# Performance work log

Measured on AMD Instinct MI355X. Metric: run time of the kernel, lower is better.

The kernel has to match this reference:

```python
import jax, jax.numpy as jnp
import numpy as np

N, E, H, NH, HD = 16384, 131072, 128, 8, 16
CUTOFF = 5.0
PATCH = H // 2  # 64, aggregation_custom effective patch dim


def setup_inputs() -> dict:
    key = jax.random.key(0)
    ks = jax.random.split(key, 24)
    w = lambda k, s: (jax.random.normal(k, s, dtype=jnp.float32) * 0.05)
    d = jax.random.normal(ks[5], (E, 3), dtype=jnp.float32)
    d = d / (jnp.linalg.norm(d, axis=-1, keepdims=True) + 1e-8)  # unit directions
    return {
        "x": jax.random.normal(ks[0], (N, H), dtype=jnp.float32),
        "vec": jax.random.normal(ks[1], (N, 3, H), dtype=jnp.float32),
        "edge_index": jax.random.randint(ks[2], (2, E), 0, N),
        "r_ij": jax.random.uniform(ks[3], (E,), dtype=jnp.float32) * CUTOFF,
        "f_ij": jax.random.normal(ks[4], (E, H), dtype=jnp.float32),
        "d_ij": d,
        "ln_g": jnp.ones((H,), jnp.float32), "ln_b": jnp.zeros((H,), jnp.float32),
        "Wq": w(ks[6], (H, H)), "bq": jnp.zeros((H,), jnp.float32),
        "Wk": w(ks[7], (H, H)), "bk": jnp.zeros((H,), jnp.float32),
        "Wv": w(ks[8], (H, H)), "bv": jnp.zeros((H,), jnp.float32),
        "Wdk": w(ks[9], (H, H)), "bdk": jnp.zeros((H,), jnp.float32),
        "Wdv": w(ks[10], (H, H)), "bdv": jnp.zeros((H,), jnp.float32),
        "Wvec": w(ks[11], (3 * H, H)),
        "Ws": w(ks[12], (2 * H, H)), "bs": jnp.zeros((2 * H,), jnp.float32),
        "Wo": w(ks[13], (3 * H, H)), "bo": jnp.zeros((3 * H,), jnp.float32),
        "Wf": w(ks[14], (H, H)), "bf": jnp.zeros((H,), jnp.float32),
        "Wwsrc": w(ks[15], (H, H)), "Wwtrg": w(ks[16], (H, H)),
        "Wagg": w(ks[17], (H, PATCH)),  # fc_all: Linear(64 -> 128, no bias)
        "agg_param": jnp.full((1,), 1e-5, dtype=jnp.float32),
    }


def _cutoff(r):
    return 0.5 * (jnp.cos(jnp.pi * r / CUTOFF) + 1.0) * (r < CUTOFF).astype(r.dtype)


def _vector_rejection(v, d):
    # v: [E,3,H], d: [E,3]
    proj = (v * d[:, :, None]).sum(axis=1, keepdims=True)  # [E,1,H]
    return v - proj * d[:, :, None]


def reference(x, vec, edge_index, r_ij, f_ij, d_ij, ln_g, ln_b,
              Wq, bq, Wk, bk, Wv, bv, Wdk, bdk, Wdv, bdv, Wvec,
              Ws, bs, Wo, bo, Wf, bf, Wwsrc, Wwtrg, Wagg, agg_param):
    silu = jax.nn.silu
    n = x.shape[0]
    # LayerNorm on x; VecLayerNorm with norm_type='none', trainable=False is identity
    mu = x.mean(-1, keepdims=True)
    var = ((x - mu) ** 2).mean(-1, keepdims=True)
    xn = (x - mu) / jnp.sqrt(var + 1e-5) * ln_g + ln_b

    q = (xn @ Wq.T + bq).reshape(n, NH, HD)
    k = (xn @ Wk.T + bk).reshape(n, NH, HD)
    v = (xn @ Wv.T + bv).reshape(n, NH, HD)
    dk = silu(f_ij @ Wdk.T + bdk).reshape(-1, NH, HD)
    dv = silu(f_ij @ Wdv.T + bdv).reshape(-1, NH, HD)

    vec1, vec2, vec3 = jnp.split(jnp.einsum('nch,oh->nco', vec, Wvec), 3, axis=-1)
    vec_dot = (vec1 * vec2).sum(axis=1)  # [N,H]

    src, dst = edge_index[0], edge_index[1]  # j, i
    # --- message ---
    attn = (q[dst] * k[src] * dk).sum(-1)                      # [E,NH]
    attn = silu(attn) * _cutoff(r_ij)[:, None]
    vmsg = (v[src] * dv * attn[:, :, None]).reshape(-1, H)     # [E,H]
    s1, s2 = jnp.split(silu(vmsg @ Ws.T + bs), 2, axis=1)
    vec_msg = vec[src] * s1[:, None, :] + s2[:, None, :] * d_ij[:, :, None]  # [E,3,H]

    # --- aggregation_custom on scalar messages ---
    e = vmsg.reshape(-1, 2, PATCH)                 # [E,2,64]
    ex = jnp.clip(jnp.einsum('epd,od->epo', e, Wagg), 0.0, 1.0)  # [E,2,128]
    gated = jnp.concatenate([(e * ex[:, :, :PATCH]).sum(1),
                             (e * ex[:, :, PATCH:]).sum(1)], axis=-1)  # [E,128]
    x_orig = jax.ops.segment_sum(vmsg, dst, num_segments=n)
    x_gate = jax.ops.segment_sum(gated, dst, num_segments=n)
    x_agg = jnp.abs(agg_param) * x_gate + x_orig
    vec_agg = jax.ops.segment_sum(vec_msg.reshape(-1, 3 * H), dst, num_segments=n).reshape(n, 3, H)

    # --- update ---
    o1, o2, o3 = jnp.split(x_agg @ Wo.T + bo, 3, axis=1)
    dx = vec_dot * o2 + o3
    dvec = vec3 * o1[:, None, :] + vec_agg

    # --- edge_update ---
    w1 = _vector_rejection(jnp.einsum('ech,oh->eco', vec[dst], Wwtrg), d_ij)
    w2 = _vector_rejection(jnp.einsum('ech,oh->eco', vec[src], Wwsrc), -d_ij)
    w_dot = (w1 * w2).sum(axis=1)  # [E,H]
    df_ij = silu(f_ij @ Wf.T + bf) * w_dot
    return dx, dvec, df_ij
```

## Files before the change

### kernel.cpp

```cpp
#include <hip/hip_runtime.h>

#define NN 16384
#define NE 131072
#define HH 128

typedef unsigned short u16;
typedef unsigned int u32;
typedef __attribute__((ext_vector_type(8))) short short8;
typedef __attribute__((ext_vector_type(4))) float f32x4;
typedef __attribute__((ext_vector_type(2))) float f32x2;
typedef __attribute__((ext_vector_type(2))) u32 u32x2;

__device__ __forceinline__ float b2f(u16 u){ u32 i=((u32)u)<<16; float f; __builtin_memcpy(&f,&i,4); return f; }
__device__ __forceinline__ u16 f2b(float f){ u32 i; __builtin_memcpy(&i,&f,4); u32 r=(i+0x7fffu+((i>>16)&1u))>>16; return (u16)r; }
__device__ __forceinline__ float blo(u32 v){ return b2f((u16)(v&0xffffu)); }
__device__ __forceinline__ float bhi(u32 v){ return b2f((u16)(v>>16)); }
__device__ __forceinline__ u32 pk(float a, float b){ return (u32)f2b(a) | ((u32)f2b(b)<<16); }
__device__ __forceinline__ float siluf(float x){ return x/(1.f+__expf(-x)); }

#define SW8(b) ((b) ^ ((((b)>>8)&7)<<4))
#define SW9(b) ((b) ^ ((((b)>>9)&7)<<4))

#define PBASE 58720256u
enum : unsigned {
  O_Wq=PBASE+0, O_Wk=PBASE+16384, O_Wv=PBASE+32768, O_Wdk=PBASE+49152,
  O_Wdv=PBASE+65536, O_Wf=PBASE+81920, O_Wwsrc=PBASE+98304, O_Wwtrg=PBASE+114688,
  O_Wvec=PBASE+131072, O_Ws=PBASE+180224, O_Wo=PBASE+212992, O_Wagg=PBASE+262144,
  O_bq=PBASE+270336, O_bk=PBASE+270464, O_bv=PBASE+270592, O_bdk=PBASE+270720,
  O_bdv=PBASE+270848, O_bs=PBASE+270976, O_bo=PBASE+271232, O_bf=PBASE+271616,
  O_lng=PBASE+271744, O_lnb=PBASE+271872, O_agg=PBASE+272000
};
#define CNT_OFF 117985280u
#define CUR_OFF 118050816u
#define SE_OFF  118116352u

struct Seg { const float* s; u32 off; u32 n; };
struct Pack { Seg d[25]; int cnt; };

__global__ __launch_bounds__(256) void k_cvt(Pack p, u16* __restrict__ base){
  int tid = blockIdx.x*blockDim.x + threadIdx.x;
  int stride = gridDim.x*blockDim.x;
  for (int s=0; s<p.cnt; ++s){
    const float* src = p.d[s].s;
    u16* dst = base + p.d[s].off;
    int n = (int)p.d[s].n, n4 = n>>2;
    const f32x4* s4 = (const f32x4*)src;
    for (int i=tid; i<n4; i+=stride){
      f32x4 v = s4[i];
      u32x2 o; o[0] = pk(v[0], v[1]); o[1] = pk(v[2], v[3]);
      *(u32x2*)(dst + 4*(size_t)i) = o;
    }
    for (int i = n4*4 + tid; i < n; i += stride) dst[i] = f2b(src[i]);
  }
}

__global__ __launch_bounds__(256) void k_hist(const int* __restrict__ ei, int* __restrict__ cnt){
  int e = blockIdx.x*256 + threadIdx.x;
  atomicAdd(&cnt[ei[NE + e]], 1);
}
__global__ __launch_bounds__(1024) void k_scan(const int* __restrict__ cnt, int* __restrict__ cur){
  __shared__ int part[1024];
  int t = threadIdx.x;
  int base = t*16;
  int local[16]; int s = 0;
#pragma unroll
// ... 5 lines not shown
    __syncthreads();
    part[t] += v;
    __syncthreads();
  }
  int run = (t>0) ? part[t-1] : 0;
#pragma unroll
  for (int k=0;k<16;++k){ cur[base+k] = run; run += local[k]; }
}
__global__ __launch_bounds__(256) void k_place(const int* __restrict__ ei, int* __restrict__ cur,
                                               int* __restrict__ se){
  int e = blockIdx.x*256 + threadIdx.x;
  int p = atomicAdd(&cur[ei[NE + e]], 1);
  se[p] = e;
}

template<int NK>
__device__ __forceinline__ f32x4 mm16(const u16* A, int lda, const u16* W, int ldw, f32x4 acc){
  int lane = threadIdx.x & 63;
  const u16* pa = A + (lane & 15)*lda + ((lane>>4)<<3);
  const u16* pw = W + (lane & 15)*ldw + ((lane>>4)<<3);
#pragma unroll
  for (int kc = 0; kc < NK; ++kc){
    short8 a = *(const short8*)(pa + kc*32);
    short8 b = *(const short8*)(pw + kc*32);
    acc = __builtin_amdgcn_mfma_f32_16x16x32_bf16(a, b, acc, 0, 0, 0);
  }
  return acc;
}

__global__ __launch_bounds__(256) void k_ln(const float* __restrict__ x, const u16* __restrict__ pb,
                                            u16* __restrict__ xn){
  int wid = threadIdx.x>>6, lane = threadIdx.x & 63;
  int n = blockIdx.x*4 + wid;
  f32x2 v = *(const f32x2*)(x + (size_t)n*HH + 2*lane);
  float a0 = v[0], a1 = v[1];
  float s = a0 + a1;
#pragma unroll
  for (int m=32; m; m>>=1) s += __shfl_xor(s, m);
  float mu = s*(1.f/128.f);
  float d0 = a0-mu, d1 = a1-mu;
  float vs = d0*d0 + d1*d1;
#pragma unroll
  for (int m=32; m; m>>=1) vs += __shfl_xor(vs, m);
  float rs = rsqrtf(vs*(1.f/128.f) + 1e-5f);
  u32 gg = *(const u32*)(pb + O_lng + 2*lane);
  u32 bb = *(const u32*)(pb + O_lnb + 2*lane);
  *(u32*)(xn + (size_t)n*HH + 2*lane) = pk(d0*rs*blo(gg)+blo(bb), d1*rs*bhi(gg)+bhi(bb));
}

__global__ __launch_bounds__(256) void k_gemm_qkv(const u16* __restrict__ xn,
    const u16* __restrict__ pb, u16* __restrict__ qkv){
  int wid = threadIdx.x>>6, lane = threadIdx.x & 63;
  int ct = blockIdx.y*4 + wid;
  int r0 = blockIdx.x*16;
  unsigned wo, bo_;
  if (ct < 8)      { wo = O_Wq; bo_ = O_bq; }
  else if (ct <16) { wo = O_Wk; bo_ = O_bk; }
  else             { wo = O_Wv; bo_ = O_bv; }
  int c0 = (ct & 7)*16;
  f32x4 acc = {0,0,0,0};
  acc = mm16<4>(xn + (size_t)r0*HH, HH, pb + wo + c0*HH, HH, acc);
  int col = ct*16 + (lane & 15);
  float bb = b2f(pb[bo_ + c0 + (lane&15)]);
#pragma unroll
  for (int j=0;j<4;++j){
    int r = r0 + ((lane>>4)<<2) + j;
    qkv[(size_t)r*384 + col] = f2b(acc[j] + bb);
  }
}

__global__ __launch_bounds__(256) void k_gemm_vec(const float* __restrict__ vecf,
    const u16* __restrict__ pb,
    u16* __restrict__ v12, u16* __restrict__ vec3, u16* __restrict__ Y){
  __shared__ u16 At[16*128];
  int tid = threadIdx.x, wid = tid>>6, lane = tid & 63;
  int r0 = blockIdx.x*16;
  {
    const float* src = vecf + (size_t)r0*HH;
    for (int i = tid*4; i < 2048; i += 1024){
      f32x4 v = *(const f32x4*)(src + i);
      u32x2 o; o[0] = pk(v[0], v[1]); o[1] = pk(v[2], v[3]);
      *(u32x2*)(At + i) = o;
    }
  }
  __syncthreads();
  for (int ct = wid; ct < 40; ct += 4){
    unsigned wo; int wc0;
    if (ct < 24)      { wo = O_Wvec;  wc0 = ct*16; }
    else if (ct < 32) { wo = O_Wwsrc; wc0 = (ct-24)*16; }
    else              { wo = O_Wwtrg; wc0 = (ct-32)*16; }
    f32x4 acc = {0,0,0,0};
    acc = mm16<4>(At, HH, pb + wo + wc0*HH, HH, acc);
    u16* dst; int ldc, dc0;
    if (ct < 16)      { dst = v12;  ldc = 256; dc0 = ct*16; }
    else if (ct < 24) { dst = vec3; ldc = 128; dc0 = (ct-16)*16; }
    else if (ct < 32) { dst = Y;    ldc = 256; dc0 = (ct-24)*16; }
    else              { dst = Y;    ldc = 256; dc0 = (ct-32)*16 + 128; }
    int col = dc0 + (lane & 15);
#pragma unroll
    for (int j=0;j<4;++j){
      int r = r0 + ((lane>>4)<<2) + j;
      dst[(size_t)r*ldc + col] = f2b(acc[j]);
    }
  }
}

__global__ __launch_bounds__(256) void k_edge(const float* __restrict__ f_ij,
    const u16* __restrict__ pb,
    const u16* __restrict__ qkv, const u16* __restrict__ Y,
    const int* __restrict__ ei, const int* __restrict__ se,
    const float* __restrict__ r_ij, const float* __restrict__ d_ij,
    const float* __restrict__ vecf, const float* __restrict__ aggf,
    float* __restrict__ df, float* __restrict__ xacc, float* __restrict__ vacc){
  __shared__ u16 fs[64*128];
  __shared__ u16 g2s[64*256];
  char* fsb  = (char*)fs;
  char* g2b  = (char*)g2s;
// ... 1 lines not shown
  int t0 = blockIdx.x*64;
  int ereg=0, dreg=0, sreg=0;
  if (lane < 16){
    ereg = se[t0 + wid*16 + lane];
    dreg = ei[NE + ereg];
    sreg = ei[ereg];
  }
#pragma unroll
  for (int pass=0; pass<8; ++pass){
    int idx = pass*256 + lane*4;
    int rloc = idx >> 7, col = idx & 127;
    int er = __shfl(ereg, rloc);
    f32x4 v = *(const f32x4*)(f_ij + (size_t)er*HH + col);
    u32x2 o; o[0]=pk(v[0],v[1]); o[1]=pk(v[2],v[3]);
    int b = (wid*16 + rloc)*256 + col*2;
    *(u32x2*)(fsb + SW8(b)) = o;
  }
  {
    int arow = wid*16 + (lane&15);
    int ab = arow*256 + ((lane>>4)<<4);
    short8 a0 = *(const short8*)(fsb + SW8(ab));
    short8 a1 = *(const short8*)(fsb + SW8(ab + 64));
    short8 a2 = *(const short8*)(fsb + SW8(ab + 128));
    short8 a3 = *(const short8*)(fsb + SW8(ab + 192));
    for (int ct=0; ct<16; ++ct){
      unsigned wo  = (ct<8) ? O_Wdk : O_Wdv;
      unsigned bo_ = (ct<8) ? O_bdk : O_bdv;
      int c0 = (ct&7)*16;
      const u16* pw = pb + wo + (size_t)(c0 + (lane&15))*HH + ((lane>>4)<<3);
      f32x4 acc = {0,0,0,0};
      acc = __builtin_amdgcn_mfma_f32_16x16x32_bf16(a0, *(const short8*)(pw),      acc, 0,0,0);
      acc = __builtin_amdgcn_mfma_f32_16x16x32_bf16(a1, *(const short8*)(pw + 32), acc, 0,0,0);
      acc = __builtin_amdgcn_mfma_f32_16x16x32_bf16(a2, *(const short8*)(pw + 64), acc, 0,0,0);
      acc = __builtin_amdgcn_mfma_f32_16x16x32_bf16(a3, *(const short8*)(pw + 96), acc, 0,0,0);
      float bb = b2f(pb[bo_ + c0 + (lane&15)]);
#pragma unroll
      for (int j=0;j<4;++j){
        int r = wid*16 + ((lane>>4)<<2) + j;
        int b = r*512 + (ct*16 + (lane&15))*2;
        *(u16*)(g2b + SW9(b)) = f2b(siluf(acc[j] + bb));
      }
    }
    f32x4 ffa[8];
#pragma unroll
    for (int cf=0; cf<8; ++cf){
      const u16* pw = pb + O_Wf + (size_t)(cf*16 + (lane&15))*HH + ((lane>>4)<<3);
      f32x4 acc = {0,0,0,0};
      acc = __builtin_amdgcn_mfma_f32_16x16x32_bf16(a0, *(const short8*)(pw),      acc, 0,0,0);
      acc = __builtin_amdgcn_mfma_f32_16x16x32_bf16(a1, *(const short8*)(pw + 32), acc, 0,0,0);
      acc = __builtin_amdgcn_mfma_f32_16x16x32_bf16(a2, *(const short8*)(pw + 64), acc, 0,0,0);
      acc = __builtin_amdgcn_mfma_f32_16x16x32_bf16(a3, *(const short8*)(pw + 96), acc, 0,0,0);
      ffa[cf] = acc;
    }
#pragma unroll
    for (int cf=0; cf<8; ++cf){
      float bb = b2f(pb[O_bf + cf*16 + (lane&15)]);
#pragma unroll
      for (int j=0;j<4;++j){
        int r = wid*16 + ((lane>>4)<<2) + j;
        int b = r*256 + (cf*16 + (lane&15))*2;
        *(u16*)(fsb + SW8(b)) = f2b(siluf(ffa[cf][j] + bb));
      }
    }
  }
  int h0 = 2*lane;
  {
    int pdst = -1; u32 qq=0, ya0=0, ya1=0, ya2=0;
    int e_c = __shfl(ereg, 0), src_c = __shfl(sreg, 0);
    u32 kk_c  = *(const u32*)(qkv + (size_t)src_c*384 + 128 + h0);
    u32 vv_c  = *(const u32*)(qkv + (size_t)src_c*384 + 256 + h0);
    u32 yb0_c = *(const u32*)(Y + ((size_t)src_c*3+0)*256 + h0);
    u32 yb1_c = *(const u32*)(Y + ((size_t)src_c*3+1)*256 + h0);
    u32 yb2_c = *(const u32*)(Y + ((size_t)src_c*3+2)*256 + h0);
    float r_c   = r_ij[e_c];
    float dc0_c = d_ij[(size_t)e_c*3+0];
    float dc1_c = d_ij[(size_t)e_c*3+1];
    float dc2_c = d_ij[(size_t)e_c*3+2];
    for (int i=0;i<16;++i){
      int e = e_c;
      u32 kk=kk_c, vv=vv_c, yb0=yb0_c, yb1=yb1_c, yb2=yb2_c;
      float r=r_c, dc0=dc0_c, dc1=dc1_c, dc2=dc2_c;
      if (i<15){
        int e_n = __shfl(ereg, i+1), src_n = __shfl(sreg, i+1);
        kk_c  = *(const u32*)(qkv + (size_t)src_n*384 + 128 + h0);
        vv_c  = *(const u32*)(qkv + (size_t)src_n*384 + 256 + h0);
        yb0_c = *(const u32*)(Y + ((size_t)src_n*3+0)*256 + h0);
        yb1_c = *(const u32*)(Y + ((size_t)src_n*3+1)*256 + h0);
        yb2_c = *(const u32*)(Y + ((size_t)src_n*3+2)*256 + h0);
        r_c   = r_ij[e_n];
        dc0_c = d_ij[(size_t)e_n*3+0];
        dc1_c = d_ij[(size_t)e_n*3+1];
        dc2_c = d_ij[(size_t)e_n*3+2];
        e_c = e_n;
      }
      int el = wid*16 + i;
      int dst = __shfl(dreg, i);
      if (dst != pdst){
        qq  = *(const u32*)(qkv + (size_t)dst*384 + h0);
        ya0 = *(const u32*)(Y + ((size_t)dst*3+0)*256 + 128 + h0);
        ya1 = *(const u32*)(Y + ((size_t)dst*3+1)*256 + 128 + h0);
        ya2 = *(const u32*)(Y + ((size_t)dst*3+2)*256 + 128 + h0);
        pdst = dst;
      }
      int bdk = el*512 + h0*2;
      u32 dk = *(const u32*)(g2b + SW9(bdk));
      u32 dv = *(const u32*)(g2b + SW9(bdk + 256));
      int bff = el*256 + h0*2;
      u32 ff = *(const u32*)(fsb + SW8(bff));
      float p = blo(qq)*blo(kk)*blo(dk) + bhi(qq)*bhi(kk)*bhi(dk);
      p += __shfl_xor(p,1); p += __shfl_xor(p,2); p += __shfl_xor(p,4);
      float cut = 0.5f*(__cosf(0.6283185307f*r)+1.f) * (r < 5.f ? 1.f : 0.f);
      float attn = siluf(p)*cut;
      float m0 = blo(vv)*blo(dv)*attn, m1 = bhi(vv)*bhi(dv)*attn;
      float ab0,ab1, ad0,ad1, bd0,bd1, ss;
      ab0 = blo(ya0)*blo(yb0); ab1 = bhi(ya0)*bhi(yb0);
      ad0 = blo(ya0)*dc0;      ad1 = bhi(ya0)*dc0;
      bd0 = blo(yb0)*dc0;      bd1 = bhi(yb0)*dc0;
      ss  = dc0*dc0;
      ab0 += blo(ya1)*blo(yb1); ab1 += bhi(ya1)*bhi(yb1);
      ad0 += blo(ya1)*dc1;      ad1 += bhi(ya1)*dc1;
      bd0 += blo(yb1)*dc1;      bd1 += bhi(yb1)*dc1;
      ss  += dc1*dc1;
      ab0 += blo(ya2)*blo(yb2); ab1 += bhi(ya2)*bhi(yb2);
      ad0 += blo(ya2)*dc2;      ad1 += bhi(ya2)*dc2;
      bd0 += blo(yb2)*dc2;      bd1 += bhi(yb2)*dc2;
      ss  += dc2*dc2;
      float t = 2.f - ss;
      f32x2 dfo; dfo[0] = blo(ff)*(ab0 - ad0*bd0*t); dfo[1] = bhi(ff)*(ab1 - ad1*bd1*t);
      *(f32x2*)(df + (size_t)e*HH + h0) = dfo;
      *(u32*)(fsb + SW8(bff)) = pk(m0, m1);
    }
  }
  float absA = fabsf(aggf[0]);
#pragma unroll
  for (int rr=0; rr<2; ++rr){
    int rt = wid*2 + rr;
    int el2 = wid*16 + 8*rr + ((lane&15)>>1);
    int pb2 = el2*256 + ((lane&15)&1)*128 + ((lane>>4)<<4);
    short8 b0 = *(const short8*)(fsb + SW8(pb2));
    short8 b1 = *(const short8*)(fsb + SW8(pb2 + 64));
    for (int ct=0; ct<8; ++ct){
      const u16* pw = pb + O_Wagg + (size_t)(ct*16 + (lane&15))*64 + ((lane>>4)<<3);
      f32x4 acc = {0,0,0,0};
      acc = __builtin_amdgcn_mfma_f32_16x16x32_bf16(b0, *(const short8*)(pw),      acc, 0,0,0);
      acc = __builtin_amdgcn_mfma_f32_16x16x32_bf16(b1, *(const short8*)(pw + 32), acc, 0,0,0);
#pragma unroll
      for (int j=0;j<4;++j){
        int r = rt*16 + ((lane>>4)<<2) + j;
        int b = r*256 + (ct*16 + (lane&15))*2;
        *(u16*)(g2b + SW8(b)) = f2b(fminf(fmaxf(acc[j],0.f),1.f));
      }
    }
  }
  {
    int rdst = -1; float xc0=0.f, xc1=0.f;
    for (int i=0;i<16;++i){
      int el = wid*16 + i;
      int dst = __shfl(dreg, i);
      if (dst != rdst){
        if (rdst >= 0){
          atomicAdd(&xacc[(size_t)rdst*HH + h0],     xc0);
          atomicAdd(&xacc[(size_t)rdst*HH + h0 + 1], xc1);
        }
        rdst = dst; xc0 = xc1 = 0.f;
      }
      int bm = el*256;
      u32 mm = *(const u32*)(fsb + SW8(bm + h0*2));
      u32 ml = *(const u32*)(fsb + SW8(bm + (h0&63)*2));
      u32 mh = *(const u32*)(fsb + SW8(bm + 128 + (h0&63)*2));
      u32 ex0 = *(const u32*)(g2b + SW8((2*el)*256 + h0*2));
      u32 ex1 = *(const u32*)(g2b + SW8((2*el+1)*256 + h0*2));
      xc0 += blo(mm) + absA*(blo(ml)*blo(ex0) + blo(mh)*blo(ex1));
      xc1 += bhi(mm) + absA*(bhi(ml)*bhi(ex0) + bhi(mh)*bhi(ex1));
    }
    if (rdst >= 0){
      atomicAdd(&xacc[(size_t)rdst*HH + h0],     xc0);
      atomicAdd(&xacc[(size_t)rdst*HH + h0 + 1], xc1);
    }
  }
  {
    int arow = wid*16 + (lane&15);
    int ab = arow*256 + ((lane>>4)<<4);
    short8 sa0 = *(const short8*)(fsb + SW8(ab));
    short8 sa1 = *(const short8*)(fsb + SW8(ab + 64));
    short8 sa2 = *(const short8*)(fsb + SW8(ab + 128));
    short8 sa3 = *(const short8*)(fsb + SW8(ab + 192));
    for (int ct=0; ct<16; ++ct){
      const u16* pw = pb + O_Ws + (size_t)(ct*16 + (lane&15))*HH + ((lane>>4)<<3);
      f32x4 acc = {0,0,0,0};
      acc = __builtin_amdgcn_mfma_f32_16x16x32_bf16(sa0, *(const short8*)(pw),      acc, 0,0,0);
      acc = __builtin_amdgcn_mfma_f32_16x16x32_bf16(sa1, *(const short8*)(pw + 32), acc, 0,0,0);
      acc = __builtin_amdgcn_mfma_f32_16x16x32_bf16(sa2, *(const short8*)(pw + 64), acc, 0,0,0);
      acc = __builtin_amdgcn_mfma_f32_16x16x32_bf16(sa3, *(const short8*)(pw + 96), acc, 0,0,0);
      float bb = b2f(pb[O_bs + ct*16 + (lane&15)]);
#pragma unroll
      for (int j=0;j<4;++j){
        int r = wid*16 + ((lane>>4)<<2) + j;
        int b = r*512 + (ct*16 + (lane&15))*2;
        *(u16*)(g2b + SW9(b)) = f2b(siluf(acc[j] + bb));
      }
    }
  }
  {
    int rdst = -1;
    float vc00=0.f,vc01=0.f, vc10=0.f,vc11=0.f, vc20=0.f,vc21=0.f;
    int e_c = __shfl(ereg, 0), src_c = __shfl(sreg, 0);
    f32x2 v0_c = *(const f32x2*)(vecf + ((size_t)src_c*3+0)*HH + h0);
    f32x2 v1_c = *(const f32x2*)(vecf + ((size_t)src_c*3+1)*HH + h0);
    f32x2 v2_c = *(const f32x2*)(vecf + ((size_t)src_c*3+2)*HH + h0);
    float dc0_c = d_ij[(size_t)e_c*3+0];
    float dc1_c = d_ij[(size_t)e_c*3+1];
    float dc2_c = d_ij[(size_t)e_c*3+2];
    for (int i=0;i<16;++i){
      f32x2 vv0=v0_c, vv1=v1_c, vv2=v2_c;
// ... 10 lines not shown
      int el = wid*16 + i;
      int dst = __shfl(dreg, i);
      if (dst != rdst){
        if (rdst >= 0){
          atomicAdd(&vacc[((size_t)rdst*3+0)*HH + h0],     vc00);
          atomicAdd(&vacc[((size_t)rdst*3+0)*HH + h0 + 1], vc01);
          atomicAdd(&vacc[((size_t)rdst*3+1)*HH + h0],     vc10);
          atomicAdd(&vacc[((size_t)rdst*3+1)*HH + h0 + 1], vc11);
          atomicAdd(&vacc[((size_t)rdst*3+2)*HH + h0],     vc20);
          atomicAdd(&vacc[((size_t)rdst*3+2)*HH + h0 + 1], vc21);
        }
        rdst = dst;
        vc00=vc01=vc10=vc11=vc20=vc21=0.f;
      }
      int bs1 = el*512 + h0*2;
      u32 s1 = *(const u32*)(g2b + SW9(bs1));
      u32 s2 = *(const u32*)(g2b + SW9(bs1 + 256));
      vc00 += vv0[0]*blo(s1) + blo(s2)*dc0;  vc01 += vv0[1]*bhi(s1) + bhi(s2)*dc0;
      vc10 += vv1[0]*blo(s1) + blo(s2)*dc1;  vc11 += vv1[1]*bhi(s1) + bhi(s2)*dc1;
      vc20 += vv2[0]*blo(s1) + blo(s2)*dc2;  vc21 += vv2[1]*bhi(s1) + bhi(s2)*dc2;
    }
    if (rdst >= 0){
      atomicAdd(&vacc[((size_t)rdst*3+0)*HH + h0],     vc00);
      atomicAdd(&vacc[((size_t)rdst*3+0)*HH + h0 + 1], vc01);
      atomicAdd(&vacc[((size_t)rdst*3+1)*HH + h0],     vc10);
      atomicAdd(&vacc[((size_t)rdst*3+1)*HH + h0 + 1], vc11);
      atomicAdd(&vacc[((size_t)rdst*3+2)*HH + h0],     vc20);
      atomicAdd(&vacc[((size_t)rdst*3+2)*HH + h0 + 1], vc21);
    }
  }
}

__global__ __launch_bounds__(256) void k_update(const float* __restrict__ xacc,
    const u16* __restrict__ pb, const u16* __restrict__ v12, const u16* __restrict__ vec3,
    const float* __restrict__ vacc,
    float* __restrict__ dx, float* __restrict__ dvec){
  int wid = threadIdx.x>>6, lane = threadIdx.x & 63;
  int ct = blockIdx.y*4 + wid;
  int r0 = blockIdx.x*16;
  int c0 = ct*16;
  f32x4 a1 = {0,0,0,0}, a2 = {0,0,0,0}, a3 = {0,0,0,0};
  const float* pa = xacc + (size_t)(r0 + (lane&15))*HH + ((lane>>4)<<3);
#pragma unroll
  for (int kc=0; kc<4; ++kc){
    f32x4 f0 = *(const f32x4*)(pa + kc*32);
    f32x4 f1 = *(const f32x4*)(pa + kc*32 + 4);
    short8 av;
    av[0]=(short)f2b(f0[0]); av[1]=(short)f2b(f0[1]); av[2]=(short)f2b(f0[2]); av[3]=(short)f2b(f0[3]);
    av[4]=(short)f2b(f1[0]); av[5]=(short)f2b(f1[1]); av[6]=(short)f2b(f1[2]); av[7]=(short)f2b(f1[3]);
    const u16* pw = pb + O_Wo + (size_t)(c0 + (lane&15))*HH + ((lane>>4)<<3) + kc*32;
    short8 b1 = *(const short8*)(pw);
    short8 b2 = *(const short8*)(pw + 128*HH);
    short8 b3 = *(const short8*)(pw + 256*HH);
    a1 = __builtin_amdgcn_mfma_f32_16x16x32_bf16(av, b1, a1, 0,0,0);
    a2 = __builtin_amdgcn_mfma_f32_16x16x32_bf16(av, b2, a2, 0,0,0);
    a3 = __builtin_amdgcn_mfma_f32_16x16x32_bf16(av, b3, a3, 0,0,0);
  }
  int h = c0 + (lane & 15);
  float bo1 = b2f(pb[O_bo + h]), bo2 = b2f(pb[O_bo + 128 + h]), bo3 = b2f(pb[O_bo + 256 + h]);
#pragma unroll
  for (int j=0;j<4;++j){
    int r = r0 + ((lane>>4)<<2) + j;
    float o1 = a1[j]+bo1, o2 = a2[j]+bo2, o3 = a3[j]+bo3;
    float vdot = 0.f;
#pragma unroll
    for (int c=0;c<3;++c){
      const u16* row = v12 + ((size_t)r*3 + c)*256;
      vdot += b2f(row[h]) * b2f(row[128 + h]);
    }
    dx[(size_t)r*HH + h] = vdot*o2 + o3;
#pragma unroll
    for (int c=0;c<3;++c){
      size_t idx = ((size_t)r*3+c)*HH + h;
      dvec[idx] = b2f(vec3[idx])*o1 + vacc[idx];
    }
  }
}

extern "C" void kernel_launch(void* const* d_in, const int* in_sizes, int n_in,
                              void* d_out, int out_size, void* d_ws, size_t ws_size,
                              hipStream_t stream){
  (void)in_sizes; (void)n_in; (void)out_size; (void)ws_size;
  const float* x     = (const float*)d_in[0];
  const float* vecf  = (const float*)d_in[1];
  const int*   ei    = (const int*)d_in[2];
  const float* r_ij  = (const float*)d_in[3];
  const float* f_ij  = (const float*)d_in[4];
  const float* d_ij  = (const float*)d_in[5];
  const float* aggf  = (const float*)d_in[28];
// ... 23 lines not shown
  add(25, O_Wwsrc,16384); add(26, O_Wwtrg,16384);
  add(18, O_Wvec, 49152); add(19, O_Ws,   32768); add(21, O_Wo,   49152);
  add(27, O_Wagg,  8192);
  add(9,  O_bq, 128); add(11, O_bk, 128); add(13, O_bv, 128); add(15, O_bdk, 128);
  add(17, O_bdv, 128); add(20, O_bs, 256); add(22, O_bo, 384); add(24, O_bf, 128);
  add(6,  O_lng, 128); add(7,  O_lnb, 128); add(28, O_agg, 1);
  p.cnt = c;

  hipMemsetAsync(ws, 0, 33554432, stream);
  hipMemsetAsync(ws + CNT_OFF, 0, 65536, stream);
  k_hist<<<dim3(NE/256), 256, 0, stream>>>(ei, cnt);
  k_scan<<<dim3(1), 1024, 0, stream>>>(cnt, cur);
  k_place<<<dim3(NE/256), 256, 0, stream>>>(ei, cur, se);
  k_cvt<<<dim3(128), 256, 0, stream>>>(p, wsu);
  k_ln<<<dim3(NN/4), 256, 0, stream>>>(x, wsu, xn);
  k_gemm_qkv<<<dim3(NN/16, 6), 256, 0, stream>>>(xn, wsu, qkv);
  k_gemm_vec<<<dim3(3*NN/16), 256, 0, stream>>>(vecf, wsu, v12, vec3, Ybuf);
  k_edge<<<dim3(NE/64), 256, 0, stream>>>(f_ij, wsu, qkv, Ybuf, ei, se, r_ij, d_ij,
                                          vecf, aggf, df, xacc, vacc);
  k_update<<<dim3(NN/16, 2), 256, 0, stream>>>(xacc, wsu, v12, vec3, vacc, dx, dvec);
}
```

Baseline: 421.2 us.

## Tile node GEMMs over 64 rows with LDS-staged inputs and register-held weights

Rewrites the three node-level GEMM kernels (qkv, vec projections, update) so each block stages 64 input rows in swizzled LDS. Each wave loads its weight fragments into registers once and reuses them across four 16-row groups. Previously each 16-row tile reloaded weights from global memory. This cuts weight traffic and block count, but launches fewer, larger blocks and uses more LDS. It also adds may_alias typedefs for type-punned loads and stores, a correctness and safety cleanup.

```diff
diff --git a/kernel.cpp b/kernel.cpp
--- a/kernel.cpp
+++ b/kernel.cpp
@@ -10,6 +10,11 @@
 typedef __attribute__((ext_vector_type(4))) float f32x4;
 typedef __attribute__((ext_vector_type(2))) float f32x2;
 typedef __attribute__((ext_vector_type(2))) u32 u32x2;
+typedef u16 __attribute__((may_alias)) u16a;
+typedef u32 __attribute__((may_alias)) u32a;
+typedef short8 __attribute__((may_alias)) short8a;
+typedef u32x2 __attribute__((may_alias)) u32x2a;
+typedef f32x4 __attribute__((may_alias)) f32x4a;
 
 __device__ __forceinline__ float b2f(u16 u){ u32 i=((u32)u)<<16; float f; __builtin_memcpy(&f,&i,4); return f; }
 __device__ __forceinline__ u16 f2b(float f){ u32 i; __builtin_memcpy(&i,&f,4); u32 r=(i+0x7fffu+((i>>16)&1u))>>16; return (u16)r; }
@@ -20,6 +25,10 @@
 
 #define SW8(b) ((b) ^ ((((b)>>8)&7)<<4))
 #define SW9(b) ((b) ^ ((((b)>>9)&7)<<4))
+__device__ __forceinline__ u32 ldsr32(const char* base, int b){ return *(const u32a*)(base + SW8(b)); }
+__device__ __forceinline__ void ldsw16(char* base, int b, u16 v){ *(u16a*)(base + SW8(b)) = v; }
+__device__ __forceinline__ short8 ldsr128(const char* base, int b){ return *(const short8a*)(base + SW8(b)); }
+__device__ __forceinline__ void ldsw64(char* base, int b, u32x2 v){ *(u32x2a*)(base + SW8(b)) = v; }
 
 #define PBASE 58720256u
 enum : unsigned {
@@ -48,7 +57,7 @@
     for (int i=tid; i<n4; i+=stride){
       f32x4 v = s4[i];
       u32x2 o; o[0] = pk(v[0], v[1]); o[1] = pk(v[2], v[3]);
-      *(u32x2*)(dst + 4*(size_t)i) = o;
+      *(u32x2a*)(dst + 4*(size_t)i) = o;
     }
     for (int i = n4*4 + tid; i < n; i += stride) dst[i] = f2b(src[i]);
   }
@@ -84,20 +93,6 @@
   se[p] = e;
 }
 
-template<int NK>
-__device__ __forceinline__ f32x4 mm16(const u16* A, int lda, const u16* W, int ldw, f32x4 acc){
-  int lane = threadIdx.x & 63;
-  const u16* pa = A + (lane & 15)*lda + ((lane>>4)<<3);
-  const u16* pw = W + (lane & 15)*ldw + ((lane>>4)<<3);
-#pragma unroll
-  for (int kc = 0; kc < NK; ++kc){
-    short8 a = *(const short8*)(pa + kc*32);
-    short8 b = *(const short8*)(pw + kc*32);
-    acc = __builtin_amdgcn_mfma_f32_16x16x32_bf16(a, b, acc, 0, 0, 0);
-  }
-  return acc;
-}
-
 __global__ __launch_bounds__(256) void k_ln(const float* __restrict__ x, const u16* __restrict__ pb,
                                             u16* __restrict__ xn){
   int wid = threadIdx.x>>6, lane = threadIdx.x & 63;
@@ -113,45 +108,69 @@
 #pragma unroll
   for (int m=32; m; m>>=1) vs += __shfl_xor(vs, m);
   float rs = rsqrtf(vs*(1.f/128.f) + 1e-5f);
-  u32 gg = *(const u32*)(pb + O_lng + 2*lane);
-  u32 bb = *(const u32*)(pb + O_lnb + 2*lane);
-  *(u32*)(xn + (size_t)n*HH + 2*lane) = pk(d0*rs*blo(gg)+blo(bb), d1*rs*bhi(gg)+bhi(bb));
-}
-
-__global__ __launch_bounds__(256) void k_gemm_qkv(const u16* __restrict__ xn,
+  u32 gg = *(const u32a*)(pb + O_lng + 2*lane);
+  u32 bb = *(const u32a*)(pb + O_lnb + 2*lane);
+  *(u32a*)(xn + (size_t)n*HH + 2*lane) = pk(d0*rs*blo(gg)+blo(bb), d1*rs*bhi(gg)+bhi(bb));
+}
+
+__global__ __launch_bounds__(256) void k_qkv64(const u16* __restrict__ xn,
     const u16* __restrict__ pb, u16* __restrict__ qkv){
-  int wid = threadIdx.x>>6, lane = threadIdx.x & 63;
-  int ct = blockIdx.y*4 + wid;
-  int r0 = blockIdx.x*16;
-  unsigned wo, bo_;
-  if (ct < 8)      { wo = O_Wq; bo_ = O_bq; }
-  else if (ct <16) { wo = O_Wk; bo_ = O_bk; }
-  else             { wo = O_Wv; bo_ = O_bv; }
-  int c0 = (ct & 7)*16;
-  f32x4 acc = {0,0,0,0};
-  acc = mm16<4>(xn + (size_t)r0*HH, HH, pb + wo + c0*HH, HH, acc);
-  int col = ct*16 + (lane & 15);
-  float bb = b2f(pb[bo_ + c0 + (lane&15)]);
-#pragma unroll
-  for (int j=0;j<4;++j){
-    int r = r0 + ((lane>>4)<<2) + j;
-    qkv[(size_t)r*384 + col] = f2b(acc[j] + bb);
-  }
-}
-
-__global__ __launch_bounds__(256) void k_gemm_vec(const float* __restrict__ vecf,
+  __shared__ u16 At[64*128];
+  char* ab_ = (char*)At;
+  int tid = threadIdx.x, wid = tid>>6, lane = tid & 63;
+  int r0 = blockIdx.x*64;
+#pragma unroll
+  for (int pass=0; pass<4; ++pass){
+    int idx = (pass*256 + tid)*8;
+    int row = idx >> 7, col = idx & 127;
+    f32x4 v = *(const f32x4a*)(xn + (size_t)(r0+row)*HH + col);
+    *(f32x4a*)(ab_ + SW8(row*256 + col*2)) = v;
+  }
+  __syncthreads();
+  for (int ct = wid; ct < 24; ct += 4){
+    unsigned wo, bo_;
+    if (ct < 8)      { wo = O_Wq; bo_ = O_bq; }
+    else if (ct <16) { wo = O_Wk; bo_ = O_bk; }
+    else             { wo = O_Wv; bo_ = O_bv; }
+    int c0 = (ct & 7)*16;
+    const u16* pw = pb + wo + (size_t)(c0 + (lane&15))*HH + ((lane>>4)<<3);
+    short8 w0 = *(const short8a*)(pw);
+    short8 w1 = *(const short8a*)(pw + 32);
+    short8 w2 = *(const short8a*)(pw + 64);
+    short8 w3 = *(const short8a*)(pw + 96);
+    float bb = b2f(pb[bo_ + c0 + (lane&15)]);
+    int col = ct*16 + (lane & 15);
+#pragma unroll
+    for (int rg=0; rg<4; ++rg){
+      int abse = (rg*16 + (lane&15))*256 + ((lane>>4)<<4);
+      f32x4 acc = {0,0,0,0};
+      acc = __builtin_amdgcn_mfma_f32_16x16x32_bf16(ldsr128(ab_, abse),       w0, acc, 0,0,0);
+      acc = __builtin_amdgcn_mfma_f32_16x16x32_bf16(ldsr128(ab_, abse + 64),  w1, acc, 0,0,0);
+      acc = __builtin_amdgcn_mfma_f32_16x16x32_bf16(ldsr128(ab_, abse + 128), w2, acc, 0,0,0);
+      acc = __builtin_amdgcn_mfma_f32_16x16x32_bf16(ldsr128(ab_, abse + 192), w3, acc, 0,0,0);
+#pragma unroll
+      for (int j=0;j<4;++j){
+        int r = r0 + rg*16 + ((lane>>4)<<2) + j;
+        qkv[(size_t)r*384 + col] = f2b(acc[j] + bb);
+      }
+    }
+  }
+}
+
+__global__ __launch_bounds__(256) void k_vec64(const float* __restrict__ vecf,
     const u16* __restrict__ pb,
     u16* __restrict__ v12, u16* __restrict__ vec3, u16* __restrict__ Y){
-  __shared__ u16 At[16*128];
+  __shared__ u16 At[64*128];
+  char* ab_ = (char*)At;
   int tid = threadIdx.x, wid = tid>>6, lane = tid & 63;
-  int r0 = blockIdx.x*16;
-  {
-    const float* src = vecf + (size_t)r0*HH;
-    for (int i = tid*4; i < 2048; i += 1024){
-      f32x4 v = *(const f32x4*)(src + i);
-      u32x2 o; o[0] = pk(v[0], v[1]); o[1] = pk(v[2], v[3]);
-      *(u32x2*)(At + i) = o;
-    }
+  int r0 = blockIdx.x*64;
+#pragma unroll
+  for (int pass=0; pass<8; ++pass){
+    int idx = pass*1024 + tid*4;
+    int row = idx >> 7, col = idx & 127;
+    f32x4 v = *(const f32x4*)(vecf + (size_t)(r0+row)*HH + col);
+    u32x2 o; o[0]=pk(v[0],v[1]); o[1]=pk(v[2],v[3]);
+    ldsw64(ab_, row*256 + col*2, o);
   }
   __syncthreads();
   for (int ct = wid; ct < 40; ct += 4){
@@ -159,8 +178,11 @@
     if (ct < 24)      { wo = O_Wvec;  wc0 = ct*16; }
     else if (ct < 32) { wo = O_Wwsrc; wc0 = (ct-24)*16; }
     else              { wo = O_Wwtrg; wc0 = (ct-32)*16; }
-    f32x4 acc = {0,0,0,0};
-    acc = mm16<4>(At, HH, pb + wo + wc0*HH, HH, acc);
+    const u16* pw = pb + wo + (size_t)(wc0 + (lane&15))*HH + ((lane>>4)<<3);
+    short8 w0 = *(const short8a*)(pw);
+    short8 w1 = *(const short8a*)(pw + 32);
+    short8 w2 = *(const short8a*)(pw + 64);
+    short8 w3 = *(const short8a*)(pw + 96);
     u16* dst; int ldc, dc0;
     if (ct < 16)      { dst = v12;  ldc = 256; dc0 = ct*16; }
     else if (ct < 24) { dst = vec3; ldc = 128; dc0 = (ct-16)*16; }
@@ -168,9 +190,18 @@
     else              { dst = Y;    ldc = 256; dc0 = (ct-32)*16 + 128; }
     int col = dc0 + (lane & 15);
 #pragma unroll
-    for (int j=0;j<4;++j){
-      int r = r0 + ((lane>>4)<<2) + j;
-      dst[(size_t)r*ldc + col] = f2b(acc[j]);
+    for (int rg=0; rg<4; ++rg){
+      int abse = (rg*16 + (lane&15))*256 + ((lane>>4)<<4);
+      f32x4 acc = {0,0,0,0};
+      acc = __builtin_amdgcn_mfma_f32_16x16x32_bf16(ldsr128(ab_, abse),       w0, acc, 0,0,0);
+      acc = __builtin_amdgcn_mfma_f32_16x16x32_bf16(ldsr128(ab_, abse + 64),  w1, acc, 0,0,0);
+      acc = __builtin_amdgcn_mfma_f32_16x16x32_bf16(ldsr128(ab_, abse + 128), w2, acc, 0,0,0);
+      acc = __builtin_amdgcn_mfma_f32_16x16x32_bf16(ldsr128(ab_, abse + 192), w3, acc, 0,0,0);
+#pragma unroll
+      for (int j=0;j<4;++j){
+        int r = r0 + rg*16 + ((lane>>4)<<2) + j;
+        dst[(size_t)r*ldc + col] = f2b(acc[j]);
+      }
     }
   }
 }
@@ -202,31 +233,31 @@
     f32x4 v = *(const f32x4*)(f_ij + (size_t)er*HH + col);
     u32x2 o; o[0]=pk(v[0],v[1]); o[1]=pk(v[2],v[3]);
     int b = (wid*16 + rloc)*256 + col*2;
-    *(u32x2*)(fsb + SW8(b)) = o;
+    *(u32x2a*)(fsb + SW8(b)) = o;
   }
   {
     int arow = wid*16 + (lane&15);
     int ab = arow*256 + ((lane>>4)<<4);
-    short8 a0 = *(const short8*)(fsb + SW8(ab));
-    short8 a1 = *(const short8*)(fsb + SW8(ab + 64));
-    short8 a2 = *(const short8*)(fsb + SW8(ab + 128));
-    short8 a3 = *(const short8*)(fsb + SW8(ab + 192));
+    short8 a0 = *(const short8a*)(fsb + SW8(ab));
+    short8 a1 = *(const short8a*)(fsb + SW8(ab + 64));
+    short8 a2 = *(const short8a*)(fsb + SW8(ab + 128));
+    short8 a3 = *(const short8a*)(fsb + SW8(ab + 192));
     for (int ct=0; ct<16; ++ct){
       unsigned wo  = (ct<8) ? O_Wdk : O_Wdv;
       unsigned bo_ = (ct<8) ? O_bdk : O_bdv;
       int c0 = (ct&7)*16;
       const u16* pw = pb + wo + (size_t)(c0 + (lane&15))*HH + ((lane>>4)<<3);
       f32x4 acc = {0,0,0,0};
-      acc = __builtin_amdgcn_mfma_f32_16x16x32_bf16(a0, *(const short8*)(pw),      acc, 0,0,0);
-      acc = __builtin_amdgcn_mfma_f32_16x16x32_bf16(a1, *(const short8*)(pw + 32), acc, 0,0,0);
-      acc = __builtin_amdgcn_mfma_f32_16x16x32_bf16(a2, *(const short8*)(pw + 64), acc, 0,0,0);
-      acc = __builtin_amdgcn_mfma_f32_16x16x32_bf16(a3, *(const short8*)(pw + 96), acc, 0,0,0);
+      acc = __builtin_amdgcn_mfma_f32_16x16x32_bf16(a0, *(const short8a*)(pw),      acc, 0,0,0);
+      acc = __builtin_amdgcn_mfma_f32_16x16x32_bf16(a1, *(const short8a*)(pw + 32), acc, 0,0,0);
+      acc = __builtin_amdgcn_mfma_f32_16x16x32_bf16(a2, *(const short8a*)(pw + 64), acc, 0,0,0);
+      acc = __builtin_amdgcn_mfma_f32_16x16x32_bf16(a3, *(const short8a*)(pw + 96), acc, 0,0,0);
       float bb = b2f(pb[bo_ + c0 + (lane&15)]);
 #pragma unroll
       for (int j=0;j<4;++j){
         int r = wid*16 + ((lane>>4)<<2) + j;
         int b = r*512 + (ct*16 + (lane&15))*2;
-        *(u16*)(g2b + SW9(b)) = f2b(siluf(acc[j] + bb));
+        *(u16a*)(g2b + SW9(b)) = f2b(siluf(acc[j] + bb));
       }
     }
     f32x4 ffa[8];
@@ -234,10 +265,10 @@
     for (int cf=0; cf<8; ++cf){
       const u16* pw = pb + O_Wf + (size_t)(cf*16 + (lane&15))*HH + ((lane>>4)<<3);
       f32x4 acc = {0,0,0,0};
-      acc = __builtin_amdgcn_mfma_f32_16x16x32_bf16(a0, *(const short8*)(pw),      acc, 0,0,0);
-      acc = __builtin_amdgcn_mfma_f32_16x16x32_bf16(a1, *(const short8*)(pw + 32), acc, 0,0,0);
-      acc = __builtin_amdgcn_mfma_f32_16x16x32_bf16(a2, *(const short8*)(pw + 64), acc, 0,0,0);
-      acc = __builtin_amdgcn_mfma_f32_16x16x32_bf16(a3, *(const short8*)(pw + 96), acc, 0,0,0);
+      acc = __builtin_amdgcn_mfma_f32_16x16x32_bf16(a0, *(const short8a*)(pw),      acc, 0,0,0);
+      acc = __builtin_amdgcn_mfma_f32_16x16x32_bf16(a1, *(const short8a*)(pw + 32), acc, 0,0,0);
+      acc = __builtin_amdgcn_mfma_f32_16x16x32_bf16(a2, *(const short8a*)(pw + 64), acc, 0,0,0);
+      acc = __builtin_amdgcn_mfma_f32_16x16x32_bf16(a3, *(const short8a*)(pw + 96), acc, 0,0,0);
       ffa[cf] = acc;
     }
 #pragma unroll
@@ -247,7 +278,7 @@
       for (int j=0;j<4;++j){
         int r = wid*16 + ((lane>>4)<<2) + j;
         int b = r*256 + (cf*16 + (lane&15))*2;
-        *(u16*)(fsb + SW8(b)) = f2b(siluf(ffa[cf][j] + bb));
+        *(u16a*)(fsb + SW8(b)) = f2b(siluf(ffa[cf][j] + bb));
       }
     }
   }
@@ -255,11 +286,11 @@
   {
     int pdst = -1; u32 qq=0, ya0=0, ya1=0, ya2=0;
     int e_c = __shfl(ereg, 0), src_c = __shfl(sreg, 0);
-    u32 kk_c  = *(const u32*)(qkv + (size_t)src_c*384 + 128 + h0);
-    u32 vv_c  = *(const u32*)(qkv + (size_t)src_c*384 + 256 + h0);
-    u32 yb0_c = *(const u32*)(Y + ((size_t)src_c*3+0)*256 + h0);
-    u32 yb1_c = *(const u32*)(Y + ((size_t)src_c*3+1)*256 + h0);
-    u32 yb2_c = *(const u32*)(Y + ((size_t)src_c*3+2)*256 + h0);
+    u32 kk_c  = *(const u32a*)(qkv + (size_t)src_c*384 + 128 + h0);
+    u32 vv_c  = *(const u32a*)(qkv + (size_t)src_c*384 + 256 + h0);
+    u32 yb0_c = *(const u32a*)(Y + ((size_t)src_c*3+0)*256 + h0);
+    u32 yb1_c = *(const u32a*)(Y + ((size_t)src_c*3+1)*256 + h0);
+    u32 yb2_c = *(const u32a*)(Y + ((size_t)src_c*3+2)*256 + h0);
     float r_c   = r_ij[e_c];
     float dc0_c = d_ij[(size_t)e_c*3+0];
     float dc1_c = d_ij[(size_t)e_c*3+1];
@@ -270,11 +301,11 @@
       float r=r_c, dc0=dc0_c, dc1=dc1_c, dc2=dc2_c;
       if (i<15){
         int e_n = __shfl(ereg, i+1), src_n = __shfl(sreg, i+1);
-        kk_c  = *(const u32*)(qkv + (size_t)src_n*384 + 128 + h0);
-        vv_c  = *(const u32*)(qkv + (size_t)src_n*384 + 256 + h0);
-        yb0_c = *(const u32*)(Y + ((size_t)src_n*3+0)*256 + h0);
-        yb1_c = *(const u32*)(Y + ((size_t)src_n*3+1)*256 + h0);
-        yb2_c = *(const u32*)(Y + ((size_t)src_n*3+2)*256 + h0);
+        kk_c  = *(const u32a*)(qkv + (size_t)src_n*384 + 128 + h0);
+        vv_c  = *(const u32a*)(qkv + (size_t)src_n*384 + 256 + h0);
+        yb0_c = *(const u32a*)(Y + ((size_t)src_n*3+0)*256 + h0);
+        yb1_c = *(const u32a*)(Y + ((size_t)src_n*3+1)*256 + h0);
+        yb2_c = *(const u32a*)(Y + ((size_t)src_n*3+2)*256 + h0);
         r_c   = r_ij[e_n];
         dc0_c = d_ij[(size_t)e_n*3+0];
         dc1_c = d_ij[(size_t)e_n*3+1];
@@ -284,17 +315,17 @@
       int el = wid*16 + i;
       int dst = __shfl(dreg, i);
       if (dst != pdst){
-        qq  = *(const u32*)(qkv + (size_t)dst*384 + h0);
-        ya0 = *(const u32*)(Y + ((size_t)dst*3+0)*256 + 128 + h0);
-        ya1 = *(const u32*)(Y + ((size_t)dst*3+1)*256 + 128 + h0);
-        ya2 = *(const u32*)(Y + ((size_t)dst*3+2)*256 + 128 + h0);
+        qq  = *(const u32a*)(qkv + (size_t)dst*384 + h0);
+        ya0 = *(const u32a*)(Y + ((size_t)dst*3+0)*256 + 128 + h0);
+        ya1 = *(const u32a*)(Y + ((size_t)dst*3+1)*256 + 128 + h0);
+        ya2 = *(const u32a*)(Y + ((size_t)dst*3+2)*256 + 128 + h0);
         pdst = dst;
       }
       int bdk = el*512 + h0*2;
-      u32 dk = *(const u32*)(g2b + SW9(bdk));
-      u32 dv = *(const u32*)(g2b + SW9(bdk + 256));
+      u32 dk = *(const u32a*)(g2b + SW9(bdk));
+      u32 dv = *(const u32a*)(g2b + SW9(bdk + 256));
       int bff = el*256 + h0*2;
-      u32 ff = *(const u32*)(fsb + SW8(bff));
+      u32 ff = *(const u32a*)(fsb + SW8(bff));
       float p = blo(qq)*blo(kk)*blo(dk) + bhi(qq)*bhi(kk)*bhi(dk);
       p += __shfl_xor(p,1); p += __shfl_xor(p,2); p += __shfl_xor(p,4);
       float cut = 0.5f*(__cosf(0.6283185307f*r)+1.f) * (r < 5.f ? 1.f : 0.f);
@@ -316,7 +347,7 @@
       float t = 2.f - ss;
       f32x2 dfo; dfo[0] = blo(ff)*(ab0 - ad0*bd0*t); dfo[1] = bhi(ff)*(ab1 - ad1*bd1*t);
       *(f32x2*)(df + (size_t)e*HH + h0) = dfo;
-      *(u32*)(fsb + SW8(bff)) = pk(m0, m1);
+      *(u32a*)(fsb + SW8(bff)) = pk(m0, m1);
     }
   }
   float absA = fabsf(aggf[0]);
@@ -325,18 +356,18 @@
     int rt = wid*2 + rr;
     int el2 = wid*16 + 8*rr + ((lane&15)>>1);
     int pb2 = el2*256 + ((lane&15)&1)*128 + ((lane>>4)<<4);
-    short8 b0 = *(const short8*)(fsb + SW8(pb2));
-    short8 b1 = *(const short8*)(fsb + SW8(pb2 + 64));
+    short8 b0 = *(const short8a*)(fsb + SW8(pb2));
+    short8 b1 = *(const short8a*)(fsb + SW8(pb2 + 64));
     for (int ct=0; ct<8; ++ct){
       const u16* pw = pb + O_Wagg + (size_t)(ct*16 + (lane&15))*64 + ((lane>>4)<<3);
       f32x4 acc = {0,0,0,0};
-      acc = __builtin_amdgcn_mfma_f32_16x16x32_bf16(b0, *(const short8*)(pw),      acc, 0,0,0);
-      acc = __builtin_amdgcn_mfma_f32_16x16x32_bf16(b1, *(const short8*)(pw + 32), acc, 0,0,0);
+      acc = __builtin_amdgcn_mfma_f32_16x16x32_bf16(b0, *(const short8a*)(pw),      acc, 0,0,0);
+      acc = __builtin_amdgcn_mfma_f32_16x16x32_bf16(b1, *(const short8a*)(pw + 32), acc, 0,0,0);
 #pragma unroll
       for (int j=0;j<4;++j){
         int r = rt*16 + ((lane>>4)<<2) + j;
         int b = r*256 + (ct*16 + (lane&15))*2;
-        *(u16*)(g2b + SW8(b)) = f2b(fminf(fmaxf(acc[j],0.f),1.f));
+        *(u16a*)(g2b + SW8(b)) = f2b(fminf(fmaxf(acc[j],0.f),1.f));
       }
     }
   }
@@ -353,11 +384,11 @@
         rdst = dst; xc0 = xc1 = 0.f;
       }
       int bm = el*256;
-      u32 mm = *(const u32*)(fsb + SW8(bm + h0*2));
-      u32 ml = *(const u32*)(fsb + SW8(bm + (h0&63)*2));
-      u32 mh = *(const u32*)(fsb + SW8(bm + 128 + (h0&63)*2));
-      u32 ex0 = *(const u32*)(g2b + SW8((2*el)*256 + h0*2));
-      u32 ex1 = *(const u32*)(g2b + SW8((2*el+1)*256 + h0*2));
+      u32 mm = *(const u32a*)(fsb + SW8(bm + h0*2));
+      u32 ml = *(const u32a*)(fsb + SW8(bm + (h0&63)*2));
+      u32 mh = *(const u32a*)(fsb + SW8(bm + 128 + (h0&63)*2));
+      u32 ex0 = *(const u32a*)(g2b + SW8((2*el)*256 + h0*2));
+      u32 ex1 = *(const u32a*)(g2b + SW8((2*el+1)*256 + h0*2));
       xc0 += blo(mm) + absA*(blo(ml)*blo(ex0) + blo(mh)*blo(ex1));
       xc1 += bhi(mm) + absA*(bhi(ml)*bhi(ex0) + bhi(mh)*bhi(ex1));
     }
@@ -369,23 +400,23 @@
   {
     int arow = wid*16 + (lane&15);
     int ab = arow*256 + ((lane>>4)<<4);
-    short8 sa0 = *(const short8*)(fsb + SW8(ab));
-    short8 sa1 = *(const short8*)(fsb + SW8(ab + 64));
-    short8 sa2 = *(const short8*)(fsb + SW8(ab + 128));
-    short8 sa3 = *(const short8*)(fsb + SW8(ab + 192));
+    short8 sa0 = *(const short8a*)(fsb + SW8(ab));
+    short8 sa1 = *(const short8a*)(fsb + SW8(ab + 64));
+    short8 sa2 = *(const short8a*)(fsb + SW8(ab + 128));
+    short8 sa3 = *(const short8a*)(fsb + SW8(ab + 192));
     for (int ct=0; ct<16; ++ct){
       const u16* pw = pb + O_Ws + (size_t)(ct*16 + (lane&15))*HH + ((lane>>4)<<3);
       f32x4 acc = {0,0,0,0};
-      acc = __builtin_amdgcn_mfma_f32_16x16x32_bf16(sa0, *(const short8*)(pw),      acc, 0,0,0);
-      acc = __builtin_amdgcn_mfma_f32_16x16x32_bf16(sa1, *(const short8*)(pw + 32), acc, 0,0,0);
-      acc = __builtin_amdgcn_mfma_f32_16x16x32_bf16(sa2, *(const short8*)(pw + 64), acc, 0,0,0);
-      acc = __builtin_amdgcn_mfma_f32_16x16x32_bf16(sa3, *(const short8*)(pw + 96), acc, 0,0,0);
+      acc = __builtin_amdgcn_mfma_f32_16x16x32_bf16(sa0, *(const short8a*)(pw),      acc, 0,0,0);
+      acc = __builtin_amdgcn_mfma_f32_16x16x32_bf16(sa1, *(const short8a*)(pw + 32), acc, 0,0,0);
+      acc = __builtin_amdgcn_mfma_f32_16x16x32_bf16(sa2, *(const short8a*)(pw + 64), acc, 0,0,0);
+      acc = __builtin_amdgcn_mfma_f32_16x16x32_bf16(sa3, *(const short8a*)(pw + 96), acc, 0,0,0);
       float bb = b2f(pb[O_bs + ct*16 + (lane&15)]);
 #pragma unroll
       for (int j=0;j<4;++j){
         int r = wid*16 + ((lane>>4)<<2) + j;
         int b = r*512 + (ct*16 + (lane&15))*2;
-        *(u16*)(g2b + SW9(b)) = f2b(siluf(acc[j] + bb));
+        *(u16a*)(g2b + SW9(b)) = f2b(siluf(acc[j] + bb));
       }
     }
   }
@@ -426,8 +457,8 @@
         vc00=vc01=vc10=vc11=vc20=vc21=0.f;
       }
       int bs1 = el*512 + h0*2;
-      u32 s1 = *(const u32*)(g2b + SW9(bs1));
-      u32 s2 = *(const u32*)(g2b + SW9(bs1 + 256));
+      u32 s1 = *(const u32a*)(g2b + SW9(bs1));
+      u32 s2 = *(const u32a*)(g2b + SW9(bs1 + 256));
       vc00 += vv0[0]*blo(s1) + blo(s2)*dc0;  vc01 += vv0[1]*bhi(s1) + bhi(s2)*dc0;
       vc10 += vv1[0]*blo(s1) + blo(s2)*dc1;  vc11 += vv1[1]*bhi(s1) + bhi(s2)*dc1;
       vc20 += vv2[0]*blo(s1) + blo(s2)*dc2;  vc21 += vv2[1]*bhi(s1) + bhi(s2)*dc2;
@@ -443,48 +474,77 @@
   }
 }
 
-__global__ __launch_bounds__(256) void k_update(const float* __restrict__ xacc,
+__global__ __launch_bounds__(256) void k_upd64(const float* __restrict__ xacc,
     const u16* __restrict__ pb, const u16* __restrict__ v12, const u16* __restrict__ vec3,
     const float* __restrict__ vacc,
     float* __restrict__ dx, float* __restrict__ dvec){
-  int wid = threadIdx.x>>6, lane = threadIdx.x & 63;
-  int ct = blockIdx.y*4 + wid;
-  int r0 = blockIdx.x*16;
-  int c0 = ct*16;
-  f32x4 a1 = {0,0,0,0}, a2 = {0,0,0,0}, a3 = {0,0,0,0};
-  const float* pa = xacc + (size_t)(r0 + (lane&15))*HH + ((lane>>4)<<3);
-#pragma unroll
-  for (int kc=0; kc<4; ++kc){
-    f32x4 f0 = *(const f32x4*)(pa + kc*32);
-    f32x4 f1 = *(const f32x4*)(pa + kc*32 + 4);
-    short8 av;
-    av[0]=(short)f2b(f0[0]); av[1]=(short)f2b(f0[1]); av[2]=(short)f2b(f0[2]); av[3]=(short)f2b(f0[3]);
-    av[4]=(short)f2b(f1[0]); av[5]=(short)f2b(f1[1]); av[6]=(short)f2b(f1[2]); av[7]=(short)f2b(f1[3]);
-    const u16* pw = pb + O_Wo + (size_t)(c0 + (lane&15))*HH + ((lane>>4)<<3) + kc*32;
-    short8 b1 = *(const short8*)(pw);
-    short8 b2 = *(const short8*)(pw + 128*HH);
-    short8 b3 = *(const short8*)(pw + 256*HH);
-    a1 = __builtin_amdgcn_mfma_f32_16x16x32_bf16(av, b1, a1, 0,0,0);
-    a2 = __builtin_amdgcn_mfma_f32_16x16x32_bf16(av, b2, a2, 0,0,0);
-    a3 = __builtin_amdgcn_mfma_f32_16x16x32_bf16(av, b3, a3, 0,0,0);
-  }
-  int h = c0 + (lane & 15);
-  float bo1 = b2f(pb[O_bo + h]), bo2 = b2f(pb[O_bo + 128 + h]), bo3 = b2f(pb[O_bo + 256 + h]);
-#pragma unroll
-  for (int j=0;j<4;++j){
-    int r = r0 + ((lane>>4)<<2) + j;
-    float o1 = a1[j]+bo1, o2 = a2[j]+bo2, o3 = a3[j]+bo3;
-    float vdot = 0.f;
-#pragma unroll
-    for (int c=0;c<3;++c){
-      const u16* row = v12 + ((size_t)r*3 + c)*256;
-      vdot += b2f(row[h]) * b2f(row[128 + h]);
-    }
-    dx[(size_t)r*HH + h] = vdot*o2 + o3;
-#pragma unroll
-    for (int c=0;c<3;++c){
-      size_t idx = ((size_t)r*3+c)*HH + h;
-      dvec[idx] = b2f(vec3[idx])*o1 + vacc[idx];
+  __shared__ u16 At[64*128];
+  char* ab_ = (char*)At;
+  int tid = threadIdx.x, wid = tid>>6, lane = tid & 63;
+  int r0 = blockIdx.x*64;
+#pragma unroll
+  for (int pass=0; pass<8; ++pass){
+    int idx = pass*1024 + tid*4;
+    int row = idx >> 7, col = idx & 127;
+    f32x4 v = *(const f32x4*)(xacc + (size_t)(r0+row)*HH + col);
+    u32x2 o; o[0]=pk(v[0],v[1]); o[1]=pk(v[2],v[3]);
+    ldsw64(ab_, row*256 + col*2, o);
+  }
+  __syncthreads();
+  for (int ct = wid; ct < 8; ct += 4){
+    int c0 = ct*16;
+    const u16* pw = pb + O_Wo + (size_t)(c0 + (lane&15))*HH + ((lane>>4)<<3);
+    short8 w10 = *(const short8a*)(pw);
+    short8 w11 = *(const short8a*)(pw + 32);
+    short8 w12 = *(const short8a*)(pw + 64);
+    short8 w13 = *(const short8a*)(pw + 96);
+    short8 w20 = *(const short8a*)(pw + 128*HH);
+    short8 w21 = *(const short8a*)(pw + 128*HH + 32);
+    short8 w22 = *(const short8a*)(pw + 128*HH + 64);
+    short8 w23 = *(const short8a*)(pw + 128*HH + 96);
+    short8 w30 = *(const short8a*)(pw + 256*HH);
+    short8 w31 = *(const short8a*)(pw + 256*HH + 32);
+    short8 w32 = *(const short8a*)(pw + 256*HH + 64);
+    short8 w33 = *(const short8a*)(pw + 256*HH + 96);
+    int h = c0 + (lane & 15);
+    float bo1 = b2f(pb[O_bo + h]), bo2 = b2f(pb[O_bo + 128 + h]), bo3 = b2f(pb[O_bo + 256 + h]);
+#pragma unroll
+    for (int rg=0; rg<4; ++rg){
+      int abse = (rg*16 + (lane&15))*256 + ((lane>>4)<<4);
+      short8 af0 = ldsr128(ab_, abse);
+      short8 af1 = ldsr128(ab_, abse + 64);
+      short8 af2 = ldsr128(ab_, abse + 128);
+      short8 af3 = ldsr128(ab_, abse + 192);
+      f32x4 a1 = {0,0,0,0}, a2 = {0,0,0,0}, a3 = {0,0,0,0};
+      a1 = __builtin_amdgcn_mfma_f32_16x16x32_bf16(af0, w10, a1, 0,0,0);
+      a1 = __builtin_amdgcn_mfma_f32_16x16x32_bf16(af1, w11, a1, 0,0,0);
+      a1 = __builtin_amdgcn_mfma_f32_16x16x32_bf16(af2, w12, a1, 0,0,0);
+      a1 = __builtin_amdgcn_mfma_f32_16x16x32_bf16(af3, w13, a1, 0,0,0);
+      a2 = __builtin_amdgcn_mfma_f32_16x16x32_bf16(af0, w20, a2, 0,0,0);
+      a2 = __builtin_amdgcn_mfma_f32_16x16x32_bf16(af1, w21, a2, 0,0,0);
+      a2 = __builtin_amdgcn_mfma_f32_16x16x32_bf16(af2, w22, a2, 0,0,0);
+      a2 = __builtin_amdgcn_mfma_f32_16x16x32_bf16(af3, w23, a2, 0,0,0);
+      a3 = __builtin_amdgcn_mfma_f32_16x16x32_bf16(af0, w30, a3, 0,0,0);
+      a3 = __builtin_amdgcn_mfma_f32_16x16x32_bf16(af1, w31, a3, 0,0,0);
+      a3 = __builtin_amdgcn_mfma_f32_16x16x32_bf16(af2, w32, a3, 0,0,0);
+      a3 = __builtin_amdgcn_mfma_f32_16x16x32_bf16(af3, w33, a3, 0,0,0);
+#pragma unroll
+      for (int j=0;j<4;++j){
+        int r = r0 + rg*16 + ((lane>>4)<<2) + j;
+        float o1 = a1[j]+bo1, o2 = a2[j]+bo2, o3 = a3[j]+bo3;
+        float vdot = 0.f;
+#pragma unroll
+        for (int c=0;c<3;++c){
+          const u16* row = v12 + ((size_t)r*3 + c)*256;
+          vdot += b2f(row[h]) * b2f(row[128 + h]);
+        }
+        dx[(size_t)r*HH + h] = vdot*o2 + o3;
+#pragma unroll
+        for (int c=0;c<3;++c){
+          size_t idx = ((size_t)r*3+c)*HH + h;
+          dvec[idx] = b2f(vec3[idx])*o1 + vacc[idx];
+        }
+      }
     }
   }
 }
@@ -538,9 +598,9 @@
   k_place<<<dim3(NE/256), 256, 0, stream>>>(ei, cur, se);
   k_cvt<<<dim3(128), 256, 0, stream>>>(p, wsu);
   k_ln<<<dim3(NN/4), 256, 0, stream>>>(x, wsu, xn);
-  k_gemm_qkv<<<dim3(NN/16, 6), 256, 0, stream>>>(xn, wsu, qkv);
-  k_gemm_vec<<<dim3(3*NN/16), 256, 0, stream>>>(vecf, wsu, v12, vec3, Ybuf);
+  k_qkv64<<<dim3(NN/64), 256, 0, stream>>>(xn, wsu, qkv);
+  k_vec64<<<dim3(3*NN/64), 256, 0, stream>>>(vecf, wsu, v12, vec3, Ybuf);
   k_edge<<<dim3(NE/64), 256, 0, stream>>>(f_ij, wsu, qkv, Ybuf, ei, se, r_ij, d_ij,
                                           vecf, aggf, df, xacc, vacc);
-  k_update<<<dim3(NN/16, 2), 256, 0, stream>>>(xacc, wsu, v12, vec3, vacc, dx, dvec);
-}
+  k_upd64<<<dim3(NN/64), 256, 0, stream>>>(xacc, wsu, v12, vec3, vacc, dx, dvec);
+}
```

Result: faster. 404.9 us (-3.9%).
